# Performance work log

Hardware: AMD Instinct MI355X
Metric: run time of the kernel (lower is better)

The kernel has to match this reference:

```python
import jax, jax.numpy as jnp
import numpy as np

COS_EPS = 1e-6      # torch CosineSimilarity eps
NORM_EPS = 1e-12    # F.normalize default eps
NUM_HEADS = 4
TOPK = 5


def setup_inputs() -> dict:
    key = jax.random.key(0)
    ks = jax.random.split(key, 12)
    B, S, D_in, D = 32, 256, 768, 1024
    N = 50000
    sc = 0.02
    return {
        "hidden": jax.random.normal(ks[0], (B, S, D_in), jnp.float32),
        "table": jax.random.normal(ks[1], (N, D), jnp.float32),
        "fc1_w": jax.random.normal(ks[2], (D, D_in), jnp.float32) * sc,
        "fc1_b": jax.random.normal(ks[3], (D,), jnp.float32) * sc,
        "q_w": jax.random.normal(ks[4], (D, D), jnp.float32) * sc,
        "q_b": jax.random.normal(ks[5], (D,), jnp.float32) * sc,
        "k_w": jax.random.normal(ks[6], (D, D), jnp.float32) * sc,
        "k_b": jax.random.normal(ks[7], (D,), jnp.float32) * sc,
        "v_w": jax.random.normal(ks[8], (D, D), jnp.float32) * sc,
        "v_b": jax.random.normal(ks[9], (D,), jnp.float32) * sc,
        "out_w": jax.random.normal(ks[10], (D, D), jnp.float32) * sc,
        "out_b": jax.random.normal(ks[11], (D,), jnp.float32) * sc,
    }


def reference(hidden, table, fc1_w, fc1_b, q_w, q_b, k_w, k_b, v_w, v_b, out_w, out_b):
    B, S, _ = hidden.shape
    D = fc1_w.shape[0]
    H = NUM_HEADS
    hd = D // H

    # fc1 over last BERT hidden states: [B,S,1024]
    x = jnp.einsum("bsi,di->bsd", hidden, fc1_w) + fc1_b

    # ---- per-sample retrieval (vectorized over batch) ----
    m = jnp.mean(x, axis=1)                       # [B,D] mean over seq
    tn = jnp.linalg.norm(table, axis=1)           # [N]
    mn = jnp.linalg.norm(m, axis=1)               # [B]
    sim = (m @ table.T) / (jnp.maximum(mn, COS_EPS)[:, None]
                           * jnp.maximum(tn, COS_EPS)[None, :])  # [B,N]
    best = jnp.argmax(sim, axis=1)                # [B] top-1 cosine match

    tab_n = table / jnp.maximum(tn, NORM_EPS)[:, None]  # L2-normalized table
    sel = tab_n[best]                             # [B,D]
    # squared euclidean distance, expanded form (avoids [B,N,D] intermediate)
    d2 = (jnp.sum(sel * sel, axis=1)[:, None]
          - 2.0 * (sel @ tab_n.T)
          + jnp.sum(tab_n * tab_n, axis=1)[None, :])  # [B,N]
    _, idx = jax.lax.top_k(-d2, TOPK)             # 5 smallest distances
    targets = table[idx]                          # [B,5,D] (unnormalized rows)

    # ---- torch.nn.MultiheadAttention(query=targets, key=x, value=x) ----
    q = (jnp.einsum("bqd,ed->bqe", targets, q_w) + q_b).reshape(B, TOPK, H, hd)
    k = (jnp.einsum("bsd,ed->bse", x, k_w) + k_b).reshape(B, S, H, hd)
    v = (jnp.einsum("bsd,ed->bse", x, v_w) + v_b).reshape(B, S, H, hd)
    scores = jnp.einsum("bqhd,bkhd->bhqk", q, k) / jnp.sqrt(jnp.asarray(hd, x.dtype))
    attn = jax.nn.softmax(scores, axis=-1)        # [B,H,5,S]
    o = jnp.einsum("bhqk,bkhd->bqhd", attn, v).reshape(B, TOPK, D)
    attn_out = jnp.einsum("bqe,de->bqd", o, out_w) + out_b  # [B,5,D]

    return jnp.sum(attn_out, axis=1)              # [B,D]
```

## Files before the change

kernel.cpp:

```cpp
#include <hip/hip_runtime.h>
#include <stdint.h>

typedef short bf16x8 __attribute__((ext_vector_type(8)));
typedef float f32x4 __attribute__((ext_vector_type(4)));

#define NROWS 50000
#define BATCH 32
#define SEQ 256
#define DIN 768
#define DMODEL 1024
#define NTOPK 5
#define DOTS_BLOCKS 782
#define TPITCH 68
#define CHUNK 64
#define NCHUNK (DMODEL / CHUNK)

__device__ inline unsigned short f2bf(float f) {
  union { float f; unsigned u; } x; x.f = f;
  unsigned u = x.u;
  unsigned r = u + 0x7fffu + ((u >> 16) & 1u);
  return (unsigned short)(r >> 16);
}
__device__ inline float bf2f(unsigned short h) {
  union { unsigned u; float f; } x; x.u = ((unsigned)h) << 16; return x.f;
}

__device__ __forceinline__ void gl_lds16(const void* g, void* l) {
  __builtin_amdgcn_global_load_lds(
      (const __attribute__((address_space(1))) unsigned int*)g,
      (__attribute__((address_space(3))) unsigned int*)l, 16, 0, 0);
}

__global__ void k_f32_to_bf16(const float* __restrict__ in, unsigned short* __restrict__ out, int n) {
  int i = (blockIdx.x * blockDim.x + threadIdx.x) * 4;
  int stride = gridDim.x * blockDim.x * 4;
  for (; i < n; i += stride) {
    float4 f = *(const float4*)(in + i);
    ushort4 o;
    o.x = f2bf(f.x); o.y = f2bf(f.y); o.z = f2bf(f.z); o.w = f2bf(f.w);
    *(ushort4*)(out + i) = o;
  }
}

__global__ void k_mean_hidden(const float* __restrict__ hidden, float* __restrict__ hm) {
  int b = blockIdx.x;
  int i = threadIdx.x;
  const float* p = hidden + (size_t)b * SEQ * DIN + i;
  float s = 0.f;
  for (int t = 0; t < SEQ; ++t) s += p[t * DIN];
  hm[b * DIN + i] = s * (1.0f / SEQ);
}

__global__ void k_sgemm_wt(const float* __restrict__ A, const float* __restrict__ W,
                           const float* __restrict__ bias, float* __restrict__ C,
                           int M, int N, int K, float beta) {
  __shared__ float A_l[32][65];
  __shared__ float W_l[64][65];
  int tid = threadIdx.x;
  int tx = tid & 63, ty = tid >> 6;
  int n0 = blockIdx.x * 64, m0 = blockIdx.y * 32;
  float acc[8] = {0.f,0.f,0.f,0.f,0.f,0.f,0.f,0.f};
  for (int k0 = 0; k0 < K; k0 += 64) {
    #pragma unroll
    for (int i = 0; i < 8; ++i) {
      int idx = tid + 256 * i; int r = idx >> 6, c = idx & 63;
      A_l[r][c] = A[(size_t)(m0 + r) * K + k0 + c];
    }
    #pragma unroll
    for (int i = 0; i < 16; ++i) {
      int idx = tid + 256 * i; int r = idx >> 6, c = idx & 63;
      W_l[r][c] = W[(size_t)(n0 + r) * K + k0 + c];
    }
    __syncthreads();
    for (int kk = 0; kk < 64; ++kk) {
      float wv = W_l[tx][kk];
      #pragma unroll
      for (int r = 0; r < 8; ++r) acc[r] += A_l[ty * 8 + r][kk] * wv;
    }
    __syncthreads();
  }
  float bv = bias[n0 + tx] * beta;
  #pragma unroll
  for (int r = 0; r < 8; ++r) C[(size_t)(m0 + ty * 8 + r) * N + n0 + tx] = acc[r] + bv;
}

__global__ __launch_bounds__(256) void k_bf16_gemm(const unsigned short* __restrict__ A,
    const unsigned short* __restrict__ W, const float* __restrict__ bias,
    unsigned short* __restrict__ C, int M, int N, int K) {
  __shared__ unsigned short As[128][32];
  __shared__ unsigned short Ws[128][32];
  int tid = threadIdx.x;
  int wave = tid >> 6, lane = tid & 63;
  int wr = wave >> 1, wc = wave & 1;
  int bm = blockIdx.y * 128, bn = blockIdx.x * 128;
  int srow = lane >> 2;
  int scol = (lane & 3) * 8;
  f32x4 acc[4][4] = {};
  for (int k0 = 0; k0 < K; k0 += 32) {
    #pragma unroll
    for (int j = 0; j < 2; ++j) {
      int r0 = wave * 32 + j * 16;
      gl_lds16(A + (size_t)(bm + r0 + srow) * K + k0 + scol, &As[r0][0]);
      gl_lds16(W + (size_t)(bn + r0 + srow) * K + k0 + scol, &Ws[r0][0]);
    }
    __syncthreads();
    bf16x8 af[4], bfr[4];
    #pragma unroll
    for (int mi = 0; mi < 4; ++mi)
      af[mi] = *(const bf16x8*)(&As[wr * 64 + mi * 16 + (lane & 15)][(lane >> 4) * 8]);
    #pragma unroll
    for (int ni = 0; ni < 4; ++ni)
      bfr[ni] = *(const bf16x8*)(&Ws[wc * 64 + ni * 16 + (lane & 15)][(lane >> 4) * 8]);
    #pragma unroll
    for (int mi = 0; mi < 4; ++mi)
      #pragma unroll
      for (int ni = 0; ni < 4; ++ni)
        acc[mi][ni] = __builtin_amdgcn_mfma_f32_16x16x32_bf16(af[mi], bfr[ni], acc[mi][ni], 0, 0, 0);
    __syncthreads();
  }
  #pragma unroll
  for (int ni = 0; ni < 4; ++ni) {
    int col = bn + wc * 64 + ni * 16 + (lane & 15);
    float bv = bias[col];
    #pragma unroll
    for (int mi = 0; mi < 4; ++mi) {
      #pragma unroll
      for (int j = 0; j < 4; ++j) {
        int row = bm + wr * 64 + mi * 16 + (lane >> 4) * 4 + j;
        C[(size_t)row * N + col] = f2bf(acc[mi][ni][j] + bv);
      }
    }
  }
}

__global__ __launch_bounds__(256, 3) void k_dots(const float* __restrict__ table,
    const float* __restrict__ vecs, float* __restrict__ norm2g,
    float* __restrict__ candv, int* __restrict__ candi, int pass1, float eps) {
  __shared__ float t_lds[64 * TPITCH];
  __shared__ float dot_lds[32][65];
  __shared__ float norm_lds[64];
  __shared__ float iv_lds[64];

  int tid = threadIdx.x;
  int wave = tid >> 6, lane = tid & 63;
  int rbase = blockIdx.x * 64;

  int srow = tid >> 2;
  int sc4 = tid & 3;
  int grow = rbase + srow;
  if (grow >= NROWS) grow = NROWS - 1;
  const float* gsrc = table + (size_t)grow * DMODEL;

  int b0 = __builtin_amdgcn_readfirstlane(wave * 8);
  const float* qb = vecs + (size_t)b0 * DMODEL;

  float acc[8] = {0.f,0.f,0.f,0.f,0.f,0.f,0.f,0.f};
  float accn = 0.f;

  for (int ch = 0; ch < NCHUNK; ++ch) {
    int k0 = ch * CHUNK;
    __syncthreads();
    #pragma unroll
    for (int i = 0; i < 4; ++i) {
      int c4 = sc4 + i * 4;
      float4 v = *(const float4*)(gsrc + k0 + c4 * 4);
      *(float4*)(&t_lds[srow * TPITCH + c4 * 4]) = v;
    }
    __syncthreads();
    #pragma unroll 2
    for (int q4 = 0; q4 < 16; ++q4) {
      float4 tv = *(const float4*)(&t_lds[lane * TPITCH + q4 * 4]);
      if (pass1 && wave == 0)
        accn += tv.x * tv.x + tv.y * tv.y + tv.z * tv.z + tv.w * tv.w;
      #pragma unroll
      for (int j = 0; j < 8; ++j) {
        float4 qv = *(const float4*)(qb + (size_t)j * DMODEL + k0 + q4 * 4);
        acc[j] += tv.x * qv.x + tv.y * qv.y + tv.z * qv.z + tv.w * qv.w;
      }
    }
  }

  __syncthreads();
  #pragma unroll
  for (int j = 0; j < 8; ++j) dot_lds[wave * 8 + j][lane] = acc[j];
  if (wave == 0 && pass1) {
    norm_lds[lane] = accn;
    int rw = rbase + lane;
    if (rw < NROWS) norm2g[rw] = accn;
  }
  __syncthreads();
  if (tid < 64) {
    int rc = rbase + tid;
    if (rc >= NROWS) rc = NROWS - 1;
    float n2 = pass1 ? norm_lds[tid] : norm2g[rc];
    iv_lds[tid] = 1.0f / fmaxf(sqrtf(n2), eps);
  }
  __syncthreads();

  if (tid < 32) {
    float tv[5]; int ti[5];
    #pragma unroll
    for (int j = 0; j < 5; ++j) { tv[j] = -3.4e38f; ti[j] = 0x7fffffff; }
    for (int r = 0; r < 64; ++r) {
      int rw = rbase + r;
      if (rw >= NROWS) break;
      float v = dot_lds[tid][r] * iv_lds[r];
      if (v > tv[4] || (v == tv[4] && rw < ti[4])) {
        tv[4] = v; ti[4] = rw;
        #pragma unroll
        for (int j = 4; j > 0; --j) {
          bool sw = (tv[j] > tv[j-1]) || (tv[j] == tv[j-1] && ti[j] < ti[j-1]);
          if (sw) {
            float fv = tv[j]; tv[j] = tv[j-1]; tv[j-1] = fv;
            int ivx = ti[j]; ti[j] = ti[j-1]; ti[j-1] = ivx;
          }
        }
      }
    }
    #pragma unroll
    for (int j = 0; j < 5; ++j) {
      candv[((size_t)blockIdx.x * 32 + tid) * 5 + j] = tv[j];
      candi[((size_t)blockIdx.x * 32 + tid) * 5 + j] = ti[j];
    }
  }
}

__global__ void k_merge(const float* __restrict__ candv, const int* __restrict__ candi,
                        int* __restrict__ out_idx, int K, int nblk) {
  int b = blockIdx.x;
  int tid = threadIdx.x;
  float tv[5]; int ti[5];
  #pragma unroll
  for (int j = 0; j < 5; ++j) { tv[j] = -3.4e38f; ti[j] = 0x7fffffff; }
  for (int blk = tid; blk < nblk; blk += 256) {
    #pragma unroll
    for (int j = 0; j < 5; ++j) {
      float v = candv[((size_t)blk * 32 + b) * 5 + j];
      int idx = candi[((size_t)blk * 32 + b) * 5 + j];
      if (v > tv[4] || (v == tv[4] && idx < ti[4])) {
        tv[4] = v; ti[4] = idx;
        #pragma unroll
        for (int jj = 4; jj > 0; --jj) {
          bool sw = (tv[jj] > tv[jj-1]) || (tv[jj] == tv[jj-1] && ti[jj] < ti[jj-1]);
          if (sw) {
            float fv = tv[jj]; tv[jj] = tv[jj-1]; tv[jj-1] = fv;
            int ivx = ti[jj]; ti[jj] = ti[jj-1]; ti[jj-1] = ivx;
          }
        }
      }
    }
  }
  __shared__ float lv[256 * 5];
  __shared__ int   li[256 * 5];
  #pragma unroll
  for (int j = 0; j < 5; ++j) { lv[tid * 5 + j] = tv[j]; li[tid * 5 + j] = ti[j]; }
  __syncthreads();
  for (int off = 128; off >= 1; off >>= 1) {
    if (tid < off) {
      float av[5], bv[5]; int ai[5], bi[5];
      #pragma unroll
      for (int j = 0; j < 5; ++j) {
        av[j] = lv[tid * 5 + j]; ai[j] = li[tid * 5 + j];
        bv[j] = lv[(tid + off) * 5 + j]; bi[j] = li[(tid + off) * 5 + j];
      }
      int pa = 0, pb = 0;
      float mv[5]; int mi[5];
      #pragma unroll
      for (int j = 0; j < 5; ++j) {
        bool ta = (av[pa] > bv[pb]) || (av[pa] == bv[pb] && ai[pa] < bi[pb]);
        if (ta) { mv[j] = av[pa]; mi[j] = ai[pa]; ++pa; }
        else    { mv[j] = bv[pb]; mi[j] = bi[pb]; ++pb; }
      }
      #pragma unroll
      for (int j = 0; j < 5; ++j) { lv[tid * 5 + j] = mv[j]; li[tid * 5 + j] = mi[j]; }
    }
    __syncthreads();
  }
  if (tid == 0) {
    for (int j = 0; j < K; ++j) out_idx[b * K + j] = li[j];
  }
}

__global__ void k_gather_sel(const float* __restrict__ table, const int* __restrict__ best,
                             float* __restrict__ sel) {
  int b = blockIdx.x, e = threadIdx.x;
  int idx = best[b];
  sel[b * DMODEL + e] = table[(size_t)idx * DMODEL + e];
}

__global__ void k_gather_targets(const float* __restrict__ table, const int* __restrict__ idx5,
                                 float* __restrict__ tg) {
  int bt = blockIdx.x, e = threadIdx.x;
  int idx = idx5[bt];
  tg[(size_t)bt * DMODEL + e] = table[(size_t)idx * DMODEL + e];
}

__global__ __launch_bounds__(256) void k_attention(const float* __restrict__ q,
    const unsigned short* __restrict__ kb, const unsigned short* __restrict__ vb,
    float* __restrict__ obuf) {
  int bt = blockIdx.x;
  int b = bt / NTOPK;
  int tid = threadIdx.x;
  __shared__ float q_l[DMODEL];
  __shared__ float sc[4][SEQ];
  #pragma unroll
  for (int j = 0; j < 4; ++j) q_l[tid + 256 * j] = q[(size_t)bt * DMODEL + tid + 256 * j];
  __syncthreads();
  {
    int s = tid;
    const unsigned short* krow = kb + ((size_t)(b * SEQ + s)) * DMODEL;
    #pragma unroll
    for (int h = 0; h < 4; ++h) {
      float d = 0.f;
      for (int dd = 0; dd < 256; dd += 8) {
        uint4 pk = *(const uint4*)(krow + h * 256 + dd);
        const unsigned short* ph = (const unsigned short*)&pk;
        #pragma unroll
        for (int j2 = 0; j2 < 8; ++j2) d += bf2f(ph[j2]) * q_l[h * 256 + dd + j2];
      }
      sc[h][s] = d * 0.0625f;
    }
  }
  __syncthreads();
  {
    int h = tid >> 6, lane = tid & 63;
    float vals[4];
    float mx = -3.4e38f;
    #pragma unroll
    for (int j = 0; j < 4; ++j) { vals[j] = sc[h][lane + 64 * j]; mx = fmaxf(mx, vals[j]); }
    #pragma unroll
    for (int o = 1; o < 64; o <<= 1) mx = fmaxf(mx, __shfl_xor(mx, o));
    float sum = 0.f;
    #pragma unroll
    for (int j = 0; j < 4; ++j) { vals[j] = expf(vals[j] - mx); sum += vals[j]; }
    #pragma unroll
    for (int o = 1; o < 64; o <<= 1) sum += __shfl_xor(sum, o);
    float rz = 1.0f / sum;
    #pragma unroll
    for (int j = 0; j < 4; ++j) sc[h][lane + 64 * j] = vals[j] * rz;
  }
  __syncthreads();
  {
    int h = tid >> 6;
    int e0 = tid * 4;
    float a0 = 0.f, a1 = 0.f, a2 = 0.f, a3 = 0.f;
    const unsigned short* vbase = vb + (size_t)(b * SEQ) * DMODEL + e0;
    for (int s = 0; s < SEQ; ++s) {
      float w = sc[h][s];
      ushort4 v4 = *(const ushort4*)(vbase + (size_t)s * DMODEL);
      a0 += w * bf2f(v4.x); a1 += w * bf2f(v4.y); a2 += w * bf2f(v4.z); a3 += w * bf2f(v4.w);
    }
    float* op = obuf + (size_t)bt * DMODEL + e0;
    op[0] = a0; op[1] = a1; op[2] = a2; op[3] = a3;
  }
}

__global__ void k_osum(const float* __restrict__ obuf, float* __restrict__ osum) {
  int g = blockIdx.x * blockDim.x + threadIdx.x;
  if (g >= BATCH * DMODEL) return;
  int b = g >> 10, e = g & 1023;
  float s = 0.f;
  #pragma unroll
  for (int t = 0; t < NTOPK; ++t) s += obuf[(size_t)(b * NTOPK + t) * DMODEL + e];
  osum[g] = s;
}

extern "C" void kernel_launch(void* const* d_in, const int* in_sizes, int n_in,
                              void* d_out, int out_size, void* d_ws, size_t ws_size,
                              hipStream_t stream) {
  const float* hidden = (const float*)d_in[0];
  const float* table  = (const float*)d_in[1];
  const float* fc1_w  = (const float*)d_in[2];
  const float* fc1_b  = (const float*)d_in[3];
  const float* q_w    = (const float*)d_in[4];
  const float* q_b    = (const float*)d_in[5];
  const float* k_w    = (const float*)d_in[6];
  const float* k_b    = (const float*)d_in[7];
  const float* v_w    = (const float*)d_in[8];
  const float* v_b    = (const float*)d_in[9];
  const float* out_w  = (const float*)d_in[10];
  const float* out_b  = (const float*)d_in[11];
  float* out = (float*)d_out;

  char* ws = (char*)d_ws;
  size_t off = 0;
  auto alloc = [&](size_t bytes) -> void* {
    void* p = ws + off;
    off += (bytes + 255) & ~(size_t)255;
    return p;
  };
  unsigned short* hid_bf  = (unsigned short*)alloc((size_t)BATCH * SEQ * DIN * 2);
  unsigned short* fc1w_bf = (unsigned short*)alloc((size_t)DMODEL * DIN * 2);
  unsigned short* kw_bf   = (unsigned short*)alloc((size_t)DMODEL * DMODEL * 2);
  unsigned short* vw_bf   = (unsigned short*)alloc((size_t)DMODEL * DMODEL * 2);
  unsigned short* x_bf    = (unsigned short*)alloc((size_t)BATCH * SEQ * DMODEL * 2);
  unsigned short* k_bf    = (unsigned short*)alloc((size_t)BATCH * SEQ * DMODEL * 2);
  unsigned short* v_bf    = (unsigned short*)alloc((size_t)BATCH * SEQ * DMODEL * 2);
  float* hm      = (float*)alloc((size_t)BATCH * DIN * 4);
  float* m       = (float*)alloc((size_t)BATCH * DMODEL * 4);
  float* sel     = (float*)alloc((size_t)BATCH * DMODEL * 4);
  float* norm2   = (float*)alloc((size_t)NROWS * 4);
  float* candv   = (float*)alloc((size_t)DOTS_BLOCKS * 32 * 5 * 4);
  int*   candi   = (int*)alloc((size_t)DOTS_BLOCKS * 32 * 5 * 4);
  int*   best    = (int*)alloc(BATCH * 4);
  int*   idx5    = (int*)alloc(BATCH * NTOPK * 4);
  float* targets = (float*)alloc((size_t)BATCH * NTOPK * DMODEL * 4);
  float* qbuf    = (float*)alloc((size_t)BATCH * NTOPK * DMODEL * 4);
  float* obuf    = (float*)alloc((size_t)BATCH * NTOPK * DMODEL * 4);
  float* osum    = (float*)alloc((size_t)BATCH * DMODEL * 4);
  (void)ws_size; (void)in_sizes; (void)n_in; (void)out_size;

  k_f32_to_bf16<<<2048, 256, 0, stream>>>(hidden, hid_bf, BATCH * SEQ * DIN);
  k_f32_to_bf16<<<768, 256, 0, stream>>>(fc1_w, fc1w_bf, DMODEL * DIN);
  k_f32_to_bf16<<<1024, 256, 0, stream>>>(k_w, kw_bf, DMODEL * DMODEL);
  k_f32_to_bf16<<<1024, 256, 0, stream>>>(v_w, vw_bf, DMODEL * DMODEL);

  k_mean_hidden<<<32, 768, 0, stream>>>(hidden, hm);
  k_sgemm_wt<<<dim3(16, 1), 256, 0, stream>>>(hm, fc1_w, fc1_b, m, 32, DMODEL, DIN, 1.0f);

  k_bf16_gemm<<<dim3(8, 64), 256, 0, stream>>>(hid_bf, fc1w_bf, fc1_b, x_bf, BATCH * SEQ, DMODEL, DIN);

  k_dots<<<DOTS_BLOCKS, 256, 0, stream>>>(table, m, norm2, candv, candi, 1, 1e-6f);
  k_merge<<<32, 256, 0, stream>>>(candv, candi, best, 1, DOTS_BLOCKS);
  k_gather_sel<<<32, 1024, 0, stream>>>(table, best, sel);

  k_dots<<<DOTS_BLOCKS, 256, 0, stream>>>(table, sel, norm2, candv, candi, 0, 1e-12f);
  k_merge<<<32, 256, 0, stream>>>(candv, candi, idx5, NTOPK, DOTS_BLOCKS);
  k_gather_targets<<<160, 1024, 0, stream>>>(table, idx5, targets);

  k_sgemm_wt<<<dim3(16, 5), 256, 0, stream>>>(targets, q_w, q_b, qbuf, BATCH * NTOPK, DMODEL, DMODEL, 1.0f);

  k_bf16_gemm<<<dim3(8, 64), 256, 0, stream>>>(x_bf, kw_bf, k_b, k_bf, BATCH * SEQ, DMODEL, DMODEL);
  k_bf16_gemm<<<dim3(8, 64), 256, 0, stream>>>(x_bf, vw_bf, v_b, v_bf, BATCH * SEQ, DMODEL, DMODEL);

  k_attention<<<160, 256, 0, stream>>>(qbuf, k_bf, v_bf, obuf);
  k_osum<<<128, 256, 0, stream>>>(obuf, osum);
  k_sgemm_wt<<<dim3(16, 1), 256, 0, stream>>>(osum, out_w, out_b, out, 32, DMODEL, DMODEL, 5.0f);
}
```

Before: 662.9 us.

## Double-buffer table tiles via async LDS loads, split mean, fuse conversions

The k_dots table scan now stages 64-float chunks with global_load_lds into two XOR-swizzled LDS buffers. It prefetches the next chunk while computing the current one, and reuses the staging buffer for the dot-product scratch. With the smaller LDS footprint, launch bounds allow 4 blocks per CU. The hidden-state mean is split into 256 partial blocks plus a reduce kernel to raise parallelism over the 25 MB read, and three weight bf16 conversions are merged into one launch. This relies on the barrier also covering completion of the async LDS loads.

```diff
diff --git a/kernel.cpp b/kernel.cpp
--- a/kernel.cpp
+++ b/kernel.cpp
@@ -11,9 +11,8 @@
 #define DMODEL 1024
 #define NTOPK 5
 #define DOTS_BLOCKS 782
-#define TPITCH 68
-#define CHUNK 64
-#define NCHUNK (DMODEL / CHUNK)
+#define CHUNKF 64
+#define NCHUNK (DMODEL / CHUNKF)
 
 __device__ inline unsigned short f2bf(float f) {
   union { float f; unsigned u; } x; x.f = f;
@@ -42,12 +41,43 @@
   }
 }
 
-__global__ void k_mean_hidden(const float* __restrict__ hidden, float* __restrict__ hm) {
+__global__ void k_f32_to_bf16_3(const float* __restrict__ i0, unsigned short* __restrict__ o0, int n0,
+                                const float* __restrict__ i1, unsigned short* __restrict__ o1, int n1,
+                                const float* __restrict__ i2, unsigned short* __restrict__ o2, int n2) {
+  int base = (blockIdx.x * blockDim.x + threadIdx.x) * 4;
+  int stride = gridDim.x * blockDim.x * 4;
+  for (int i = base; i < n0; i += stride) {
+    float4 f = *(const float4*)(i0 + i);
+    ushort4 o; o.x = f2bf(f.x); o.y = f2bf(f.y); o.z = f2bf(f.z); o.w = f2bf(f.w);
+    *(ushort4*)(o0 + i) = o;
+  }
+  for (int i = base; i < n1; i += stride) {
+    float4 f = *(const float4*)(i1 + i);
+    ushort4 o; o.x = f2bf(f.x); o.y = f2bf(f.y); o.z = f2bf(f.z); o.w = f2bf(f.w);
+    *(ushort4*)(o1 + i) = o;
+  }
+  for (int i = base; i < n2; i += stride) {
+    float4 f = *(const float4*)(i2 + i);
+    ushort4 o; o.x = f2bf(f.x); o.y = f2bf(f.y); o.z = f2bf(f.z); o.w = f2bf(f.w);
+    *(ushort4*)(o2 + i) = o;
+  }
+}
+
+__global__ void k_mean_part(const float* __restrict__ hidden, float* __restrict__ hpart) {
+  int b = blockIdx.x >> 3, tc = blockIdx.x & 7;
+  int i = threadIdx.x;
+  const float* p = hidden + ((size_t)b * SEQ + tc * 32) * DIN + i;
+  float s = 0.f;
+  #pragma unroll 4
+  for (int t = 0; t < 32; ++t) s += p[t * DIN];
+  hpart[((size_t)tc * 32 + b) * DIN + i] = s;
+}
+__global__ void k_mean_reduce(const float* __restrict__ hpart, float* __restrict__ hm) {
   int b = blockIdx.x;
   int i = threadIdx.x;
-  const float* p = hidden + (size_t)b * SEQ * DIN + i;
   float s = 0.f;
-  for (int t = 0; t < SEQ; ++t) s += p[t * DIN];
+  #pragma unroll
+  for (int tc = 0; tc < 8; ++tc) s += hpart[((size_t)tc * 32 + b) * DIN + i];
   hm[b * DIN + i] = s * (1.0f / SEQ);
 }
 
@@ -133,43 +163,48 @@
   }
 }
 
-__global__ __launch_bounds__(256, 3) void k_dots(const float* __restrict__ table,
+__global__ __launch_bounds__(256, 4) void k_dots(const float* __restrict__ table,
     const float* __restrict__ vecs, float* __restrict__ norm2g,
     float* __restrict__ candv, int* __restrict__ candi, int pass1, float eps) {
-  __shared__ float t_lds[64 * TPITCH];
-  __shared__ float dot_lds[32][65];
+  __shared__ float t_lds[2][64 * 64];
   __shared__ float norm_lds[64];
   __shared__ float iv_lds[64];
+  float* dot_lds = &t_lds[0][0];
 
   int tid = threadIdx.x;
   int wave = tid >> 6, lane = tid & 63;
   int rbase = blockIdx.x * 64;
 
-  int srow = tid >> 2;
-  int sc4 = tid & 3;
-  int grow = rbase + srow;
-  if (grow >= NROWS) grow = NROWS - 1;
-  const float* gsrc = table + (size_t)grow * DMODEL;
-
   int b0 = __builtin_amdgcn_readfirstlane(wave * 8);
   const float* qb = vecs + (size_t)b0 * DMODEL;
 
+  int u = lane & 15;
+  int rsub = lane >> 4;
+
   float acc[8] = {0.f,0.f,0.f,0.f,0.f,0.f,0.f,0.f};
   float accn = 0.f;
 
+  auto STAGE = [&](int buf, int k0) {
+    #pragma unroll
+    for (int j = 0; j < 4; ++j) {
+      int rl = wave * 16 + j * 4 + rsub;
+      int gr = rbase + rl; if (gr >= NROWS) gr = NROWS - 1;
+      int c = ((u & 7) ^ (rl & 7)) | (u & 8);
+      gl_lds16(table + (size_t)gr * DMODEL + k0 + c * 4,
+               &t_lds[buf][(wave * 16 + j * 4) * 64]);
+    }
+  };
+
+  STAGE(0, 0);
+  __syncthreads();
+  int cur = 0;
   for (int ch = 0; ch < NCHUNK; ++ch) {
-    int k0 = ch * CHUNK;
-    __syncthreads();
-    #pragma unroll
-    for (int i = 0; i < 4; ++i) {
-      int c4 = sc4 + i * 4;
-      float4 v = *(const float4*)(gsrc + k0 + c4 * 4);
-      *(float4*)(&t_lds[srow * TPITCH + c4 * 4]) = v;
-    }
-    __syncthreads();
+    int k0 = ch * CHUNKF;
+    if (ch + 1 < NCHUNK) STAGE(cur ^ 1, k0 + CHUNKF);
     #pragma unroll 2
     for (int q4 = 0; q4 < 16; ++q4) {
-      float4 tv = *(const float4*)(&t_lds[lane * TPITCH + q4 * 4]);
+      int uu = ((q4 & 7) ^ (lane & 7)) | (q4 & 8);
+      float4 tv = *(const float4*)(&t_lds[cur][lane * 64 + uu * 4]);
       if (pass1 && wave == 0)
         accn += tv.x * tv.x + tv.y * tv.y + tv.z * tv.z + tv.w * tv.w;
       #pragma unroll
@@ -178,15 +213,18 @@
         acc[j] += tv.x * qv.x + tv.y * qv.y + tv.z * qv.z + tv.w * qv.w;
       }
     }
-  }
-
-  __syncthreads();
-  #pragma unroll
-  for (int j = 0; j < 8; ++j) dot_lds[wave * 8 + j][lane] = acc[j];
-  if (wave == 0 && pass1) {
+    __syncthreads();
+    cur ^= 1;
+  }
+
+  #pragma unroll
+  for (int j = 0; j < 8; ++j) dot_lds[(wave * 8 + j) * 66 + lane] = acc[j];
+  if (wave == 0) {
     norm_lds[lane] = accn;
-    int rw = rbase + lane;
-    if (rw < NROWS) norm2g[rw] = accn;
+    if (pass1) {
+      int rw = rbase + lane;
+      if (rw < NROWS) norm2g[rw] = accn;
+    }
   }
   __syncthreads();
   if (tid < 64) {
@@ -204,7 +242,7 @@
     for (int r = 0; r < 64; ++r) {
       int rw = rbase + r;
       if (rw >= NROWS) break;
-      float v = dot_lds[tid][r] * iv_lds[r];
+      float v = dot_lds[tid * 66 + r] * iv_lds[r];
       if (v > tv[4] || (v == tv[4] && rw < ti[4])) {
         tv[4] = v; ti[4] = rw;
         #pragma unroll
@@ -396,6 +434,7 @@
   unsigned short* x_bf    = (unsigned short*)alloc((size_t)BATCH * SEQ * DMODEL * 2);
   unsigned short* k_bf    = (unsigned short*)alloc((size_t)BATCH * SEQ * DMODEL * 2);
   unsigned short* v_bf    = (unsigned short*)alloc((size_t)BATCH * SEQ * DMODEL * 2);
+  float* hpart   = (float*)alloc((size_t)8 * BATCH * DIN * 4);
   float* hm      = (float*)alloc((size_t)BATCH * DIN * 4);
   float* m       = (float*)alloc((size_t)BATCH * DMODEL * 4);
   float* sel     = (float*)alloc((size_t)BATCH * DMODEL * 4);
@@ -411,11 +450,12 @@
   (void)ws_size; (void)in_sizes; (void)n_in; (void)out_size;
 
   k_f32_to_bf16<<<2048, 256, 0, stream>>>(hidden, hid_bf, BATCH * SEQ * DIN);
-  k_f32_to_bf16<<<768, 256, 0, stream>>>(fc1_w, fc1w_bf, DMODEL * DIN);
-  k_f32_to_bf16<<<1024, 256, 0, stream>>>(k_w, kw_bf, DMODEL * DMODEL);
-  k_f32_to_bf16<<<1024, 256, 0, stream>>>(v_w, vw_bf, DMODEL * DMODEL);
-
-  k_mean_hidden<<<32, 768, 0, stream>>>(hidden, hm);
+  k_f32_to_bf16_3<<<1024, 256, 0, stream>>>(fc1_w, fc1w_bf, DMODEL * DIN,
+                                            k_w, kw_bf, DMODEL * DMODEL,
+                                            v_w, vw_bf, DMODEL * DMODEL);
+
+  k_mean_part<<<256, 768, 0, stream>>>(hidden, hpart);
+  k_mean_reduce<<<32, 768, 0, stream>>>(hpart, hm);
   k_sgemm_wt<<<dim3(16, 1), 256, 0, stream>>>(hm, fc1_w, fc1_b, m, 32, DMODEL, DIN, 1.0f);
 
   k_bf16_gemm<<<dim3(8, 64), 256, 0, stream>>>(hid_bf, fc1w_bf, fc1_b, x_bf, BATCH * SEQ, DMODEL, DIN);
```

After: 644.2 us. 1.03x faster.
